# Kernel tuning notes

Hardware: AMD Instinct MI355X
Metric: run time of the kernel (lower is better)

## Reference

```python
import jax, jax.numpy as jnp
import numpy as np

B, S, H, NH, HD = 2, 2048, 4096, 32, 128
NEG = jnp.finfo(jnp.float32).min


def rotate_half(x):
    x1, x2 = x[..., : x.shape[-1] // 2], x[..., x.shape[-1] // 2 :]
    return jnp.concatenate((-x2, x1), axis=-1)


def setup_inputs() -> dict:
    key = jax.random.key(0)
    ks = jax.random.split(key, 7)
    return {
        "hidden_states": jax.random.normal(ks[0], (B, S, H), jnp.float32),
        "cos": jax.random.uniform(ks[1], (1, 1, S, HD), jnp.float32),
        "sin": jax.random.uniform(ks[2], (1, 1, S, HD), jnp.float32),
        "Wq": jax.random.normal(ks[3], (H, H), jnp.float32) * 0.02,
        "Wk": jax.random.normal(ks[4], (HD, H), jnp.float32) * 0.02,
        "Wv": jax.random.normal(ks[5], (HD, H), jnp.float32) * 0.02,
        "Wd": jax.random.normal(ks[6], (H, H), jnp.float32) * 0.02,
    }


def reference(hidden_states, cos, sin, Wq, Wk, Wv, Wd):
    b, s, _ = hidden_states.shape
    q = (hidden_states @ Wq.T).reshape(b, s, NH, HD).transpose(0, 2, 1, 3)  # [B,NH,S,HD]
    k = (hidden_states @ Wk.T)[:, None, :, :]  # [B,1,S,HD] (multi-query)
    v = (hidden_states @ Wv.T)[:, None, :, :]
    # inline RoPE
    q = q * cos + rotate_half(q) * sin
    k = k * cos + rotate_half(k) * sin
    scale = 1.0 / jnp.sqrt(jnp.float32(HD))
    scores = jnp.einsum("bhqd,bhkd->bhqk", q, k) * scale
    # causal mask: additive finfo.min above diagonal
    causal = jnp.tril(jnp.ones((s, s), jnp.bool_))
    scores = scores + jnp.where(causal, 0.0, NEG)
    attn = jax.nn.softmax(scores, axis=-1)
    out = jnp.einsum("bhqk,bhkd->bhqd", attn, v)  # [B,NH,S,HD]
    out = out.transpose(0, 2, 1, 3).reshape(b, s, NH * HD)
    return out @ Wd.T
```

## Files before the change

kernel.cpp:

```cpp
#include <hip/hip_runtime.h>
#include <hip/hip_bf16.h>
#include <math.h>

constexpr int Bc  = 2;
constexpr int Sc  = 2048;
constexpr int Hc  = 4096;
constexpr int NHc = 32;
constexpr int HDc = 128;

typedef __attribute__((ext_vector_type(8))) __bf16 bf16x8;
typedef __attribute__((ext_vector_type(4))) __bf16 bf16x4;
typedef __attribute__((ext_vector_type(4))) float  f32x4;

#if defined(__has_builtin)
#if __has_builtin(__builtin_amdgcn_global_load_lds)
#define HAS_GLL 1
#endif
#endif
#ifndef HAS_GLL
#define HAS_GLL 0
#endif

__device__ __forceinline__ float fast_exp2(float x) {
#if defined(__has_builtin)
#if __has_builtin(__builtin_amdgcn_exp2f)
    return __builtin_amdgcn_exp2f(x);
#else
    return exp2f(x);
#endif
#else
    return exp2f(x);
#endif
}

#define CFENCE asm volatile("" ::: "memory")
#define BARRIER do { CFENCE; __builtin_amdgcn_s_barrier(); CFENCE; } while (0)
#define WAITVM(n) asm volatile("s_waitcnt vmcnt(" #n ")" ::: "memory")

__device__ __forceinline__ void gll16(const __bf16* g, __bf16* lds_base, int lane) {
#if HAS_GLL
    __builtin_amdgcn_global_load_lds((const __attribute__((address_space(1))) void*)g,
                                     (__attribute__((address_space(3))) void*)lds_base,
                                     16, 0, 0);
#else
    *(int4*)(lds_base + lane * 8) = *(const int4*)g;
#endif
}

__global__ void cvt_f32_bf16(const float* __restrict__ in, __bf16* __restrict__ out, int n) {
    int i = (blockIdx.x * blockDim.x + threadIdx.x) * 4;
    if (i >= n) return;
    const float4 v = *(const float4*)(in + i);
    bf16x4 o;
    o[0] = (__bf16)v.x; o[1] = (__bf16)v.y; o[2] = (__bf16)v.z; o[3] = (__bf16)v.w;
    *(bf16x4*)(out + i) = o;
}

__global__ void prep(const float* __restrict__ hs, const float* __restrict__ Wq,
                     const float* __restrict__ Wk, const float* __restrict__ Wv,
                     __bf16* __restrict__ hs16, __bf16* __restrict__ wq16,
                     __bf16* __restrict__ wkv16) {
    const int blk = blockIdx.x;
    if (blk < 16384) {
        int i = (blk * 256 + threadIdx.x) * 4;
        const float4 v = *(const float4*)(hs + i);
        bf16x4 o;
        o[0] = (__bf16)v.x; o[1] = (__bf16)v.y; o[2] = (__bf16)v.z; o[3] = (__bf16)v.w;
        *(bf16x4*)(hs16 + i) = o;
    } else if (blk < 32768) {
        int i = ((blk - 16384) * 256 + threadIdx.x) * 4;
        const float4 v = *(const float4*)(Wq + i);
        bf16x4 o;
        o[0] = (__bf16)v.x; o[1] = (__bf16)v.y; o[2] = (__bf16)v.z; o[3] = (__bf16)v.w;
        *(bf16x4*)(wq16 + i) = o;
    } else {
        int i = ((blk - 32768) * 256 + threadIdx.x) * 4;
        int row = i >> 12;
        int col = i & (Hc - 1);
        const float* src = (row < HDc) ? (Wk + (long)row * Hc + col)
                                       : (Wv + (long)(row - HDc) * Hc + col);
        const float4 v = *(const float4*)src;
        bf16x4 o;
        o[0] = (__bf16)v.x; o[1] = (__bf16)v.y; o[2] = (__bf16)v.z; o[3] = (__bf16)v.w;
        *(bf16x4*)(wkv16 + i) = o;
    }
}

template <typename OUT>
__global__ __launch_bounds__(512, 2)
void gemm256(const __bf16* __restrict__ A, const __bf16* __restrict__ B,
             OUT* __restrict__ C, int M, int N, int K) {
    __shared__ __bf16 As[2][256 * 64];
    __shared__ __bf16 Bs[2][256 * 64];

    const int tid  = threadIdx.x;
    const int wave = tid >> 6, lane = tid & 63;
    const int lrow = lane & 15, quad = lane >> 4;
    const int wm = wave >> 2, wn = wave & 3;

    const int nwg = gridDim.x * gridDim.y;
    const int bid = blockIdx.y * gridDim.x + blockIdx.x;
    const int wg  = (bid & 7) * (nwg >> 3) + (bid >> 3);
    const int m0  = (wg / gridDim.x) * 256;
    const int n0  = (wg % gridDim.x) * 256;

    f32x4 acc[8][4] = {};

    int srow[4][2], sbase[4][2];
    const int rp   = lane >> 3;
    const int scol = ((lane & 7) ^ rp) << 3;
#pragma unroll
    for (int it = 0; it < 2; ++it) {
        const int c   = wave * 2 + it;
        const int rb0 = (c < 8) ? c * 8 : 128 + (c - 8) * 8;
        const int rb1 = (c >> 2) * 64 + (c & 3) * 8;
        srow[0][it] = rb0 + rp;       sbase[0][it] = rb0 * 64;
        srow[1][it] = rb1 + rp;       sbase[1][it] = rb1 * 64;
        srow[2][it] = rb1 + 32 + rp;  sbase[2][it] = (rb1 + 32) * 64;
        srow[3][it] = rb0 + 64 + rp;  sbase[3][it] = (rb0 + 64) * 64;
    }
    const __bf16* Ab = A + (long)m0 * K;
    const __bf16* Bb = B + (long)n0 * K;

    auto stageg = [&](int g, int bu, long k0) {
        const __bf16* gb = (g == 0 || g == 3) ? Ab : Bb;
        __bf16* lb = (g == 0 || g == 3) ? &As[bu][0] : &Bs[bu][0];
#pragma unroll
        for (int it = 0; it < 2; ++it)
            gll16(gb + (long)srow[g][it] * K + k0 + scol, lb + sbase[g][it], lane);
    };

    const int fc0  = ((quad ^ (lrow & 7)) << 3);
    const int fc1  = (((4 | quad) ^ (lrow & 7)) << 3);
    const int arow = wm * 128 + lrow;
    const int brow = wn * 64 + lrow;

    const int nk = K >> 6;
    stageg(0, 0, 0); stageg(1, 0, 0); stageg(2, 0, 0); stageg(3, 0, 0);
    WAITVM(4);
    BARRIER;

    for (int kt = 0; kt < nk; ++kt) {
        const int bu = kt & 1;
        const bool more = (kt + 1 < nk);
        const long k1 = (long)(kt + 1) * 64;
        bf16x8 af[2][4], bv0[2][2], bv1[2][2];

#pragma unroll
        for (int i2 = 0; i2 < 4; ++i2) {
            af[0][i2] = *(const bf16x8*)&As[bu][(arow + i2 * 16) * 64 + fc0];
            af[1][i2] = *(const bf16x8*)&As[bu][(arow + i2 * 16) * 64 + fc1];
        }
#pragma unroll
        for (int j2 = 0; j2 < 2; ++j2) {
            bv0[0][j2] = *(const bf16x8*)&Bs[bu][(brow + j2 * 16) * 64 + fc0];
            bv0[1][j2] = *(const bf16x8*)&Bs[bu][(brow + j2 * 16) * 64 + fc1];
        }
        if (more) { stageg(0, bu ^ 1, k1); WAITVM(4); } else { WAITVM(0); }
        BARRIER;
        __builtin_amdgcn_s_setprio(1);
#pragma unroll
        for (int c = 0; c < 2; ++c)
#pragma unroll
            for (int i2 = 0; i2 < 4; ++i2)
#pragma unroll
                for (int j2 = 0; j2 < 2; ++j2)
                    acc[i2][j2] = __builtin_amdgcn_mfma_f32_16x16x32_bf16(
                        af[c][i2], bv0[c][j2], acc[i2][j2], 0, 0, 0);
        __builtin_amdgcn_s_setprio(0);
        BARRIER;

#pragma unroll
        for (int j2 = 0; j2 < 2; ++j2) {
            bv1[0][j2] = *(const bf16x8*)&Bs[bu][(brow + 32 + j2 * 16) * 64 + fc0];
            bv1[1][j2] = *(const bf16x8*)&Bs[bu][(brow + 32 + j2 * 16) * 64 + fc1];
        }
        if (more) { stageg(1, bu ^ 1, k1); WAITVM(4); } else { WAITVM(0); }
        BARRIER;
        __builtin_amdgcn_s_setprio(1);
#pragma unroll
        for (int c = 0; c < 2; ++c)
#pragma unroll
            for (int i2 = 0; i2 < 4; ++i2)
#pragma unroll
                for (int j2 = 0; j2 < 2; ++j2)
                    acc[i2][2 + j2] = __builtin_amdgcn_mfma_f32_16x16x32_bf16(
                        af[c][i2], bv1[c][j2], acc[i2][2 + j2], 0, 0, 0);
        __builtin_amdgcn_s_setprio(0);
        BARRIER;

#pragma unroll
        for (int i2 = 0; i2 < 4; ++i2) {
            af[0][i2] = *(const bf16x8*)&As[bu][(arow + 64 + i2 * 16) * 64 + fc0];
            af[1][i2] = *(const bf16x8*)&As[bu][(arow + 64 + i2 * 16) * 64 + fc1];
        }
        if (more) { stageg(2, bu ^ 1, k1); WAITVM(4); } else { WAITVM(0); }
        BARRIER;
        __builtin_amdgcn_s_setprio(1);
#pragma unroll
        for (int c = 0; c < 2; ++c)
#pragma unroll
            for (int i2 = 0; i2 < 4; ++i2)
#pragma unroll
                for (int j2 = 0; j2 < 2; ++j2)
                    acc[4 + i2][j2] = __builtin_amdgcn_mfma_f32_16x16x32_bf16(
                        af[c][i2], bv0[c][j2], acc[4 + i2][j2], 0, 0, 0);
        __builtin_amdgcn_s_setprio(0);
        BARRIER;

        if (more) { stageg(3, bu ^ 1, k1); WAITVM(4); } else { WAITVM(0); }
        BARRIER;
        __builtin_amdgcn_s_setprio(1);
#pragma unroll
        for (int c = 0; c < 2; ++c)
#pragma unroll
            for (int i2 = 0; i2 < 4; ++i2)
#pragma unroll
                for (int j2 = 0; j2 < 2; ++j2)
                    acc[4 + i2][2 + j2] = __builtin_amdgcn_mfma_f32_16x16x32_bf16(
                        af[c][i2], bv1[c][j2], acc[4 + i2][2 + j2], 0, 0, 0);
        __builtin_amdgcn_s_setprio(0);
        BARRIER;
    }

#pragma unroll
    for (int i = 0; i < 8; ++i) {
        const int row = m0 + wm * 128 + i * 16 + quad * 4;
#pragma unroll
        for (int j = 0; j < 4; ++j) {
            const int col = n0 + wn * 64 + j * 16 + lrow;
            OUT* cp = C + (long)row * N + col;
#pragma unroll
            for (int r = 0; r < 4; ++r) cp[(long)r * N] = (OUT)acc[i][j][r];
        }
    }
}

template <typename OUT>
__global__ __launch_bounds__(256)
void gemm_bt64(const __bf16* __restrict__ A, const __bf16* __restrict__ B,
               OUT* __restrict__ C, int M, int N, int K) {
    __shared__ __bf16 As[2][64][64];
    __shared__ __bf16 Bs[2][64][64];

    const int tid  = threadIdx.x;
    const int wave = tid >> 6, lane = tid & 63;
    const int lrow = lane & 15, quad = lane >> 4;
    const int m0   = blockIdx.y * 64;
    const int n0   = blockIdx.x * 64;
    const int wr   = (wave >> 1) * 32;
    const int wc   = (wave & 1) * 32;

    f32x4 acc[2][2] = {};

    int srow[2], scol[2];
#pragma unroll
    for (int it = 0; it < 2; ++it) {
        int e = (wave * 2 + it) * 1024 + lane * 16;
        int r = e >> 7;
        int cb = (e >> 4) & 7;
        srow[it] = r;
        scol[it] = ((cb ^ (r & 7)) * 8);
    }
    const __bf16* Ab = A + (long)m0 * K;
    const __bf16* Bb = B + (long)n0 * K;

    auto stage = [&](int kt, int bu) {
        const long k0 = (long)kt * 64;
#pragma unroll
        for (int it = 0; it < 2; ++it)
            gll16(Ab + (long)srow[it] * K + k0 + scol[it], &As[bu][0][0] + (wave * 2 + it) * 512, lane);
#pragma unroll
        for (int it = 0; it < 2; ++it)
            gll16(Bb + (long)srow[it] * K + k0 + scol[it], &Bs[bu][0][0] + (wave * 2 + it) * 512, lane);
    };

    const int fcol0 = ((quad ^ (lrow & 7)) << 3);
    const int fcol1 = (((4 | quad) ^ (lrow & 7)) << 3);

    const int nk = K >> 6;
    stage(0, 0);
    for (int kt = 0; kt < nk; ++kt) {
        __syncthreads();
        if (kt + 1 < nk) stage(kt + 1, (kt + 1) & 1);
        const int bu = kt & 1;

#pragma unroll
        for (int c = 0; c < 2; ++c) {
            const int fc = c ? fcol1 : fcol0;
            bf16x8 af[2], bfv[2];
#pragma unroll
            for (int i = 0; i < 2; ++i) af[i]  = *(const bf16x8*)&As[bu][wr + i * 16 + lrow][fc];
#pragma unroll
            for (int j = 0; j < 2; ++j) bfv[j] = *(const bf16x8*)&Bs[bu][wc + j * 16 + lrow][fc];
#pragma unroll
            for (int i = 0; i < 2; ++i)
#pragma unroll
                for (int j = 0; j < 2; ++j)
                    acc[i][j] = __builtin_amdgcn_mfma_f32_16x16x32_bf16(af[i], bfv[j], acc[i][j], 0, 0, 0);
        }
    }

#pragma unroll
    for (int i = 0; i < 2; ++i) {
        const int row = m0 + wr + i * 16 + quad * 4;
#pragma unroll
        for (int j = 0; j < 2; ++j) {
            const int col = n0 + wc + j * 16 + lrow;
            OUT* cp = C + (long)row * N + col;
#pragma unroll
            for (int r = 0; r < 4; ++r) cp[(long)r * N] = (OUT)acc[i][j][r];
        }
    }
}

__global__ void ropek_vtrans(__bf16* __restrict__ KV, const float* __restrict__ cosb,
                             const float* __restrict__ sinb, __bf16* __restrict__ Vt) {
    __shared__ __bf16 T[128][72];
    const int tid = threadIdx.x;
    if (blockIdx.x < 128) {
        int gid  = blockIdx.x * 256 + tid;
        int row  = gid >> 3;
        int dblk = (gid & 7) * 8;
        int s    = row & (Sc - 1);
        __bf16* p = KV + (long)row * 256;
        const float* cp = cosb + s * HDc;
        const float* sp = sinb + s * HDc;
        bf16x8 lo = *(bf16x8*)(p + dblk);
        bf16x8 hi = *(bf16x8*)(p + dblk + 64);
        bf16x8 olo, ohi;
#pragma unroll
        for (int j = 0; j < 8; ++j) {
            float ql = (float)lo[j], qh = (float)hi[j];
            float cl = cp[dblk + j],      sl = sp[dblk + j];
            float ch = cp[dblk + 64 + j], sh = sp[dblk + 64 + j];
            olo[j] = (__bf16)(ql * cl - qh * sl);
            ohi[j] = (__bf16)(qh * ch + ql * sh);
        }
        *(bf16x8*)(p + dblk)      = olo;
        *(bf16x8*)(p + dblk + 64) = ohi;
    } else {
        const int vb = blockIdx.x - 128;
        const int s0 = (vb & (Sc / 64 - 1)) * 64;
        const int b  = vb / (Sc / 64);
#pragma unroll
        for (int i = 0; i < 4; ++i) {
            int e = i * 256 + tid;
            int s = e >> 4, dc = (e & 15) * 8;
            bf16x8 v = *(const bf16x8*)(KV + (long)(b * Sc + s0 + s) * 256 + 128 + dc);
#pragma unroll
            for (int j = 0; j < 8; ++j) T[dc + j][s] = v[j];
        }
        __syncthreads();
#pragma unroll
        for (int i = 0; i < 4; ++i) {
            int e = i * 256 + tid;
            int d = e >> 3, sc8 = (e & 7) * 8;
            bf16x8 v;
#pragma unroll
            for (int j = 0; j < 8; ++j) v[j] = T[d][sc8 + j];
            *(bf16x8*)(Vt + (long)(b * HDc + d) * Sc + s0 + sc8) = v;
        }
    }
}

__global__ __launch_bounds__(256, 2)
void attn(const __bf16* __restrict__ Q,
          const __bf16* __restrict__ KV,
          const __bf16* __restrict__ Vt,
          const float* __restrict__ cosb,
          const float* __restrict__ sinb,
          __bf16* __restrict__ O) {
    const int qt   = (gridDim.x - 1) - blockIdx.x;
    const int bh   = blockIdx.y;
    const int b    = bh >> 5, h = bh & 31;
    const int tid  = threadIdx.x;
    const int wave = tid >> 6, lane = tid & 63;
    const int lrow = lane & 15, quad = lane >> 4;

    __shared__ __bf16 Ks[2][64][128];
    __shared__ __bf16 Vs[2][128][64];
    __shared__ __bf16 Ps[4][16][72];

    bf16x8 vone;
#pragma unroll
    for (int j = 0; j < 8; ++j) vone[j] = (__bf16)1.0f;

    const int q0 = qt * 128 + wave * 32;

    const float qscale = 0.08838834764831845f * 1.4426950408889634f;
    bf16x8 aq[2][4];
#pragma unroll
    for (int qq = 0; qq < 2; ++qq) {
        const int s = q0 + qq * 16 + lrow;
        const __bf16* qp = Q + (long)(b * Sc + s) * Hc + h * HDc + quad * 8;
        const float* cp = cosb + s * HDc + quad * 8;
        const float* sp = sinb + s * HDc + quad * 8;
        bf16x8 raw[4];
#pragma unroll
        for (int c = 0; c < 4; ++c) raw[c] = *(const bf16x8*)(qp + c * 32);
#pragma unroll
        for (int c = 0; c < 2; ++c) {
#pragma unroll
            for (int j = 0; j < 8; ++j) {
                const int d = c * 32 + j;
                float ql = (float)raw[c][j], qh = (float)raw[c + 2][j];
                float cl = cp[d],      sl = sp[d];
                float ch = cp[d + 64], sh = sp[d + 64];
                aq[qq][c][j]     = (__bf16)((ql * cl - qh * sl) * qscale);
                aq[qq][c + 2][j] = (__bf16)((qh * ch + ql * sh) * qscale);
            }
        }
    }

    f32x4 o[2][8] = {};
    f32x4 lac[2] = {};
    float mst[2][4];
#pragma unroll
    for (int qq = 0; qq < 2; ++qq)
#pragma unroll
        for (int r = 0; r < 4; ++r) mst[qq][r] = -3.0e38f;

    const __bf16* kvb = KV + (long)b * Sc * 256;
    const __bf16* vtb = Vt + (long)b * HDc * Sc;
    int krow[4], kcol[4], vrow[4], vcol[4];
#pragma unroll
    for (int it = 0; it < 4; ++it) {
        int e = (wave * 4 + it) * 1024 + lane * 16;
        int rk = e >> 8, cbk = (e >> 4) & 15;
        krow[it] = rk; kcol[it] = ((cbk ^ (rk & 15)) * 8);
        int rv = e >> 7, cbv = (e >> 4) & 7;
        vrow[it] = rv; vcol[it] = ((cbv ^ (rv & 7)) * 8);
    }

    auto stage = [&](int kt, int bu) {
#pragma unroll
        for (int it = 0; it < 4; ++it) {
            gll16(kvb + (long)(kt * 64 + krow[it]) * 256 + kcol[it],
                  &Ks[bu][0][0] + (wave * 4 + it) * 512, lane);
            gll16(vtb + (long)vrow[it] * Sc + kt * 64 + vcol[it],
                  &Vs[bu][0][0] + (wave * 4 + it) * 512, lane);
        }
    };

    const int nt = 2 * qt + 2;
    stage(0, 0);

    for (int kt = 0; kt < nt; ++kt) {
        __syncthreads();
        if (kt + 1 < nt) stage(kt + 1, (kt + 1) & 1);
        const int bu = kt & 1;

        f32x4 sc[2][4] = {};
        __builtin_amdgcn_s_setprio(1);
#pragma unroll
        for (int ct = 0; ct < 4; ++ct) {
#pragma unroll
            for (int c = 0; c < 4; ++c) {
                bf16x8 bk = *(const bf16x8*)&Ks[bu][ct * 16 + lrow][(((c << 2) | quad) ^ lrow) << 3];
                sc[0][ct] = __builtin_amdgcn_mfma_f32_16x16x32_bf16(aq[0][c], bk, sc[0][ct], 0, 0, 0);
                sc[1][ct] = __builtin_amdgcn_mfma_f32_16x16x32_bf16(aq[1][c], bk, sc[1][ct], 0, 0, 0);
            }
        }
        __builtin_amdgcn_s_setprio(0);

        bf16x8 ap[2][2];
#pragma unroll
        for (int qq = 0; qq < 2; ++qq) {
            if (kt * 64 + 63 > q0 + qq * 16) {
#pragma unroll
                for (int ct = 0; ct < 4; ++ct) {
                    int kv = kt * 64 + ct * 16 + lrow;
#pragma unroll
                    for (int r = 0; r < 4; ++r) {
                        int qr = q0 + qq * 16 + quad * 4 + r;
                        if (kv > qr) sc[qq][ct][r] = -3.0e38f;
                    }
                }
            }

            float lmax[4];
#pragma unroll
            for (int r = 0; r < 4; ++r)
                lmax[r] = fmaxf(fmaxf(sc[qq][0][r], sc[qq][1][r]),
                                fmaxf(sc[qq][2][r], sc[qq][3][r]));
            const bool near_ok = (lmax[0] <= mst[qq][0] + 8.0f) &&
                                 (lmax[1] <= mst[qq][1] + 8.0f) &&
                                 (lmax[2] <= mst[qq][2] + 8.0f) &&
                                 (lmax[3] <= mst[qq][3] + 8.0f);
            if (!__all(near_ok)) {
                float alf[4];
#pragma unroll
                for (int r = 0; r < 4; ++r) {
                    float mx = lmax[r];
#pragma unroll
                    for (int off = 1; off < 16; off <<= 1) mx = fmaxf(mx, __shfl_xor(mx, off, 64));
                    float mnew = fmaxf(mst[qq][r], mx);
                    alf[r]     = fast_exp2(mst[qq][r] - mnew);
                    mst[qq][r] = mnew;
                }
#pragma unroll
                for (int dt = 0; dt < 8; ++dt)
#pragma unroll
                    for (int r = 0; r < 4; ++r) o[qq][dt][r] *= alf[r];
#pragma unroll
                for (int r = 0; r < 4; ++r) lac[qq][r] *= alf[r];
            }
#pragma unroll
            for (int ct = 0; ct < 4; ++ct)
#pragma unroll
                for (int r = 0; r < 4; ++r)
                    sc[qq][ct][r] = fast_exp2(sc[qq][ct][r] - mst[qq][r]);

#pragma unroll
            for (int ct = 0; ct < 4; ++ct)
#pragma unroll
                for (int r = 0; r < 4; ++r)
                    Ps[wave][quad * 4 + r][ct * 16 + lrow] = (__bf16)sc[qq][ct][r];
#pragma unroll
            for (int ks = 0; ks < 2; ++ks)
                ap[qq][ks] = *(const bf16x8*)&Ps[wave][lrow][ks * 32 + quad * 8];
        }

        __builtin_amdgcn_s_setprio(1);
#pragma unroll
        for (int dt = 0; dt < 8; ++dt) {
#pragma unroll
            for (int ks = 0; ks < 2; ++ks) {
                bf16x8 bv = *(const bf16x8*)&Vs[bu][dt * 16 + lrow]
                                [(((ks << 2) | quad) ^ (lrow & 7)) << 3];
#pragma unroll
                for (int qq = 0; qq < 2; ++qq)
                    o[qq][dt] = __builtin_amdgcn_mfma_f32_16x16x32_bf16(ap[qq][ks], bv, o[qq][dt], 0, 0, 0);
            }
        }
#pragma unroll
        for (int ks = 0; ks < 2; ++ks) {
#pragma unroll
            for (int qq = 0; qq < 2; ++qq)
                lac[qq] = __builtin_amdgcn_mfma_f32_16x16x32_bf16(ap[qq][ks], vone, lac[qq], 0, 0, 0);
        }
        __builtin_amdgcn_s_setprio(0);
    }

#pragma unroll
    for (int qq = 0; qq < 2; ++qq)
#pragma unroll
        for (int r = 0; r < 4; ++r) {
            float inv = 1.f / lac[qq][r];
            int qr = q0 + qq * 16 + quad * 4 + r;
            __bf16* op = O + (long)(b * Sc + qr) * Hc + h * HDc;
#pragma unroll
            for (int dt = 0; dt < 8; ++dt) op[dt * 16 + lrow] = (__bf16)(o[qq][dt][r] * inv);
        }
}

extern "C" void kernel_launch(void* const* d_in, const int* in_sizes, int n_in,
                              void* d_out, int out_size, void* d_ws, size_t ws_size,
                              hipStream_t stream) {
    const float* hs   = (const float*)d_in[0];
    const float* cosb = (const float*)d_in[1];
    const float* sinb = (const float*)d_in[2];
    const float* Wq   = (const float*)d_in[3];
    const float* Wk   = (const float*)d_in[4];
    const float* Wv   = (const float*)d_in[5];
    const float* Wd   = (const float*)d_in[6];
    float* out = (float*)d_out;

    char* ws = (char*)d_ws;
    const long SZ_HS  = (long)Bc * Sc * Hc * 2;
    const long SZ_W   = (long)Hc * Hc * 2;
    const long SZ_KV  = (long)Bc * Sc * 256 * 2;
    __bf16* hs16  = (__bf16*)(ws);
    __bf16* wq16  = (__bf16*)(ws + SZ_HS);
    __bf16* wkv16 = (__bf16*)(ws + SZ_HS + SZ_W);
    __bf16* q16   = (__bf16*)(ws + SZ_HS + SZ_W + SZ_KV);
    __bf16* kv16  = (__bf16*)(ws + SZ_HS + SZ_W + SZ_KV + SZ_HS);
    __bf16* vt16  = (__bf16*)(ws + SZ_HS + SZ_W + SZ_KV + SZ_HS + SZ_KV);
    __bf16* att16 = hs16;
    __bf16* wd16  = wq16;

    const int nW  = Hc * Hc;

    prep<<<33792, 256, 0, stream>>>(hs, Wq, Wk, Wv, hs16, wq16, wkv16);

    gemm256<__bf16><<<dim3(Hc / 256, (Bc * Sc) / 256), 512, 0, stream>>>(
        hs16, wq16, q16, Bc * Sc, Hc, Hc);
    gemm_bt64<__bf16><<<dim3(256 / 64, (Bc * Sc) / 64), 256, 0, stream>>>(
        hs16, wkv16, kv16, Bc * Sc, 256, Hc);

    cvt_f32_bf16<<<nW / 1024, 256, 0, stream>>>(Wd, wd16, nW);

    ropek_vtrans<<<128 + Bc * (Sc / 64), 256, 0, stream>>>(kv16, cosb, sinb, vt16);

    attn<<<dim3(Sc / 128, Bc * NHc), 256, 0, stream>>>(q16, kv16, vt16, cosb, sinb, att16);

    gemm256<float><<<dim3(Hc / 256, (Bc * Sc) / 256), 512, 0, stream>>>(
        att16, wd16, out, Bc * Sc, Hc, Hc);
}
```

Baseline: 654.6 us.

## Fuse Q and KV projections into one 256-tile GEMM and fold Wd cast into prep

The separate small-tile KV projection GEMM is merged into the large-tile Q GEMM by appending the 256 KV output columns as an extra N-tile column, with per-block output pointer and stride selection. When the workspace is large enough, Wd is converted to bf16 inside the prep kernel into its own buffer instead of a separate launch that reuses the Wq buffer. This removes two launches and the poorly-occupied 64x64 GEMM. The cost is a grid of 17 N-tiles that the swizzle remapping may handle unevenly, plus extra workspace.

After: 741.4 us. 1.13x slower.

```diff
diff --git a/kernel.cpp b/kernel.cpp
--- a/kernel.cpp
+++ b/kernel.cpp
@@ -58,8 +58,9 @@
 
 __global__ void prep(const float* __restrict__ hs, const float* __restrict__ Wq,
                      const float* __restrict__ Wk, const float* __restrict__ Wv,
+                     const float* __restrict__ Wd,
                      __bf16* __restrict__ hs16, __bf16* __restrict__ wq16,
-                     __bf16* __restrict__ wkv16) {
+                     __bf16* __restrict__ wkv16, __bf16* __restrict__ wd16) {
     const int blk = blockIdx.x;
     if (blk < 16384) {
         int i = (blk * 256 + threadIdx.x) * 4;
@@ -73,7 +74,7 @@
         bf16x4 o;
         o[0] = (__bf16)v.x; o[1] = (__bf16)v.y; o[2] = (__bf16)v.z; o[3] = (__bf16)v.w;
         *(bf16x4*)(wq16 + i) = o;
-    } else {
+    } else if (blk < 33792) {
         int i = ((blk - 32768) * 256 + threadIdx.x) * 4;
         int row = i >> 12;
         int col = i & (Hc - 1);
@@ -83,13 +84,19 @@
         bf16x4 o;
         o[0] = (__bf16)v.x; o[1] = (__bf16)v.y; o[2] = (__bf16)v.z; o[3] = (__bf16)v.w;
         *(bf16x4*)(wkv16 + i) = o;
-    }
-}
-
-template <typename OUT>
+    } else {
+        int i = ((blk - 33792) * 256 + threadIdx.x) * 4;
+        const float4 v = *(const float4*)(Wd + i);
+        bf16x4 o;
+        o[0] = (__bf16)v.x; o[1] = (__bf16)v.y; o[2] = (__bf16)v.z; o[3] = (__bf16)v.w;
+        *(bf16x4*)(wd16 + i) = o;
+    }
+}
+
 __global__ __launch_bounds__(512, 2)
-void gemm256(const __bf16* __restrict__ A, const __bf16* __restrict__ B,
-             OUT* __restrict__ C, int M, int N, int K) {
+void gemm_qkv(const __bf16* __restrict__ A, const __bf16* __restrict__ Wq16,
+              const __bf16* __restrict__ Wkv16, __bf16* __restrict__ Qo,
+              __bf16* __restrict__ KVo, int M, int K) {
     __shared__ __bf16 As[2][256 * 64];
     __shared__ __bf16 Bs[2][256 * 64];
 
@@ -120,7 +127,8 @@
         srow[3][it] = rb0 + 64 + rp;  sbase[3][it] = (rb0 + 64) * 64;
     }
     const __bf16* Ab = A + (long)m0 * K;
-    const __bf16* Bb = B + (long)n0 * K;
+    const __bf16* Bb = (n0 < Hc) ? (Wq16 + (long)n0 * K)
+                                 : (Wkv16 + (long)(n0 - Hc) * K);
 
     auto stageg = [&](int g, int bu, long k0) {
         const __bf16* gb = (g == 0 || g == 3) ? Ab : Bb;
@@ -223,90 +231,165 @@
         BARRIER;
     }
 
+    const long ldc  = (n0 < Hc) ? Hc : 256;
+    const int  nloc = (n0 < Hc) ? n0 : n0 - Hc;
+    __bf16* Cb = (n0 < Hc) ? Qo : KVo;
 #pragma unroll
     for (int i = 0; i < 8; ++i) {
         const int row = m0 + wm * 128 + i * 16 + quad * 4;
 #pragma unroll
         for (int j = 0; j < 4; ++j) {
-            const int col = n0 + wn * 64 + j * 16 + lrow;
-            OUT* cp = C + (long)row * N + col;
-#pragma unroll
-            for (int r = 0; r < 4; ++r) cp[(long)r * N] = (OUT)acc[i][j][r];
+            const int col = nloc + wn * 64 + j * 16 + lrow;
+            __bf16* cp = Cb + (long)row * ldc + col;
+#pragma unroll
+            for (int r = 0; r < 4; ++r) cp[(long)r * ldc] = (__bf16)acc[i][j][r];
         }
     }
 }
 
 template <typename OUT>
-__global__ __launch_bounds__(256)
-void gemm_bt64(const __bf16* __restrict__ A, const __bf16* __restrict__ B,
-               OUT* __restrict__ C, int M, int N, int K) {
-    __shared__ __bf16 As[2][64][64];
-    __shared__ __bf16 Bs[2][64][64];
+__global__ __launch_bounds__(512, 2)
+void gemm256(const __bf16* __restrict__ A, const __bf16* __restrict__ B,
+             OUT* __restrict__ C, int M, int N, int K) {
+    __shared__ __bf16 As[2][256 * 64];
+    __shared__ __bf16 Bs[2][256 * 64];
 
     const int tid  = threadIdx.x;
     const int wave = tid >> 6, lane = tid & 63;
     const int lrow = lane & 15, quad = lane >> 4;
-    const int m0   = blockIdx.y * 64;
-    const int n0   = blockIdx.x * 64;
-    const int wr   = (wave >> 1) * 32;
-    const int wc   = (wave & 1) * 32;
-
-    f32x4 acc[2][2] = {};
-
-    int srow[2], scol[2];
+    const int wm = wave >> 2, wn = wave & 3;
+
+    const int nwg = gridDim.x * gridDim.y;
+    const int bid = blockIdx.y * gridDim.x + blockIdx.x;
+    const int wg  = (bid & 7) * (nwg >> 3) + (bid >> 3);
+    const int m0  = (wg / gridDim.x) * 256;
+    const int n0  = (wg % gridDim.x) * 256;
+
+    f32x4 acc[8][4] = {};
+
+    int srow[4][2], sbase[4][2];
+    const int rp   = lane >> 3;
+    const int scol = ((lane & 7) ^ rp) << 3;
 #pragma unroll
     for (int it = 0; it < 2; ++it) {
-        int e = (wave * 2 + it) * 1024 + lane * 16;
-        int r = e >> 7;
-        int cb = (e >> 4) & 7;
-        srow[it] = r;
-        scol[it] = ((cb ^ (r & 7)) * 8);
+        const int c   = wave * 2 + it;
+        const int rb0 = (c < 8) ? c * 8 : 128 + (c - 8) * 8;
+        const int rb1 = (c >> 2) * 64 + (c & 3) * 8;
+        srow[0][it] = rb0 + rp;       sbase[0][it] = rb0 * 64;
+        srow[1][it] = rb1 + rp;       sbase[1][it] = rb1 * 64;
+        srow[2][it] = rb1 + 32 + rp;  sbase[2][it] = (rb1 + 32) * 64;
+        srow[3][it] = rb0 + 64 + rp;  sbase[3][it] = (rb0 + 64) * 64;
     }
     const __bf16* Ab = A + (long)m0 * K;
     const __bf16* Bb = B + (long)n0 * K;
 
-    auto stage = [&](int kt, int bu) {
-        const long k0 = (long)kt * 64;
+    auto stageg = [&](int g, int bu, long k0) {
+        const __bf16* gb = (g == 0 || g == 3) ? Ab : Bb;
+        __bf16* lb = (g == 0 || g == 3) ? &As[bu][0] : &Bs[bu][0];
 #pragma unroll
         for (int it = 0; it < 2; ++it)
-            gll16(Ab + (long)srow[it] * K + k0 + scol[it], &As[bu][0][0] + (wave * 2 + it) * 512, lane);
-#pragma unroll
-        for (int it = 0; it < 2; ++it)
-            gll16(Bb + (long)srow[it] * K + k0 + scol[it], &Bs[bu][0][0] + (wave * 2 + it) * 512, lane);
+            gll16(gb + (long)srow[g][it] * K + k0 + scol, lb + sbase[g][it], lane);
     };
 
-    const int fcol0 = ((quad ^ (lrow & 7)) << 3);
-    const int fcol1 = (((4 | quad) ^ (lrow & 7)) << 3);
+    const int fc0  = ((quad ^ (lrow & 7)) << 3);
+    const int fc1  = (((4 | quad) ^ (lrow & 7)) << 3);
+    const int arow = wm * 128 + lrow;
+    const int brow = wn * 64 + lrow;
 
     const int nk = K >> 6;
-    stage(0, 0);
+    stageg(0, 0, 0); stageg(1, 0, 0); stageg(2, 0, 0); stageg(3, 0, 0);
+    WAITVM(4);
+    BARRIER;
+
     for (int kt = 0; kt < nk; ++kt) {
-        __syncthreads();
-        if (kt + 1 < nk) stage(kt + 1, (kt + 1) & 1);
         const int bu = kt & 1;
-
-#pragma unroll
-        for (int c = 0; c < 2; ++c) {
-            const int fc = c ? fcol1 : fcol0;
-            bf16x8 af[2], bfv[2];
-#pragma unroll
-            for (int i = 0; i < 2; ++i) af[i]  = *(const bf16x8*)&As[bu][wr + i * 16 + lrow][fc];
-#pragma unroll
-            for (int j = 0; j < 2; ++j) bfv[j] = *(const bf16x8*)&Bs[bu][wc + j * 16 + lrow][fc];
-#pragma unroll
-            for (int i = 0; i < 2; ++i)
-#pragma unroll
-                for (int j = 0; j < 2; ++j)
-                    acc[i][j] = __builtin_amdgcn_mfma_f32_16x16x32_bf16(af[i], bfv[j], acc[i][j], 0, 0, 0);
-        }
-    }
-
-#pragma unroll
-    for (int i = 0; i < 2; ++i) {
-        const int row = m0 + wr + i * 16 + quad * 4;
-#pragma unroll
-        for (int j = 0; j < 2; ++j) {
-            const int col = n0 + wc + j * 16 + lrow;
+        const bool more = (kt + 1 < nk);
+        const long k1 = (long)(kt + 1) * 64;
+        bf16x8 af[2][4], bv0[2][2], bv1[2][2];
+
+#pragma unroll
+        for (int i2 = 0; i2 < 4; ++i2) {
+            af[0][i2] = *(const bf16x8*)&As[bu][(arow + i2 * 16) * 64 + fc0];
+            af[1][i2] = *(const bf16x8*)&As[bu][(arow + i2 * 16) * 64 + fc1];
+        }
+#pragma unroll
+        for (int j2 = 0; j2 < 2; ++j2) {
+            bv0[0][j2] = *(const bf16x8*)&Bs[bu][(brow + j2 * 16) * 64 + fc0];
+            bv0[1][j2] = *(const bf16x8*)&Bs[bu][(brow + j2 * 16) * 64 + fc1];
+        }
+        if (more) { stageg(0, bu ^ 1, k1); WAITVM(4); } else { WAITVM(0); }
+        BARRIER;
+        __builtin_amdgcn_s_setprio(1);
+#pragma unroll
+        for (int c = 0; c < 2; ++c)
+#pragma unroll
+            for (int i2 = 0; i2 < 4; ++i2)
+#pragma unroll
+                for (int j2 = 0; j2 < 2; ++j2)
+                    acc[i2][j2] = __builtin_amdgcn_mfma_f32_16x16x32_bf16(
+                        af[c][i2], bv0[c][j2], acc[i2][j2], 0, 0, 0);
+        __builtin_amdgcn_s_setprio(0);
+        BARRIER;
+
+#pragma unroll
+        for (int j2 = 0; j2 < 2; ++j2) {
+            bv1[0][j2] = *(const bf16x8*)&Bs[bu][(brow + 32 + j2 * 16) * 64 + fc0];
+            bv1[1][j2] = *(const bf16x8*)&Bs[bu][(brow + 32 + j2 * 16) * 64 + fc1];
+        }
+        if (more) { stageg(1, bu ^ 1, k1); WAITVM(4); } else { WAITVM(0); }
+        BARRIER;
+        __builtin_amdgcn_s_setprio(1);
+#pragma unroll
+        for (int c = 0; c < 2; ++c)
+#pragma unroll
+            for (int i2 = 0; i2 < 4; ++i2)
+#pragma unroll
+                for (int j2 = 0; j2 < 2; ++j2)
+                    acc[i2][2 + j2] = __builtin_amdgcn_mfma_f32_16x16x32_bf16(
+                        af[c][i2], bv1[c][j2], acc[i2][2 + j2], 0, 0, 0);
+        __builtin_amdgcn_s_setprio(0);
+        BARRIER;
+
+#pragma unroll
+        for (int i2 = 0; i2 < 4; ++i2) {
+            af[0][i2] = *(const bf16x8*)&As[bu][(arow + 64 + i2 * 16) * 64 + fc0];
+            af[1][i2] = *(const bf16x8*)&As[bu][(arow + 64 + i2 * 16) * 64 + fc1];
+        }
+        if (more) { stageg(2, bu ^ 1, k1); WAITVM(4); } else { WAITVM(0); }
+        BARRIER;
+        __builtin_amdgcn_s_setprio(1);
+#pragma unroll
+        for (int c = 0; c < 2; ++c)
+#pragma unroll
+            for (int i2 = 0; i2 < 4; ++i2)
+#pragma unroll
+                for (int j2 = 0; j2 < 2; ++j2)
+                    acc[4 + i2][j2] = __builtin_amdgcn_mfma_f32_16x16x32_bf16(
+                        af[c][i2], bv0[c][j2], acc[4 + i2][j2], 0, 0, 0);
+        __builtin_amdgcn_s_setprio(0);
+        BARRIER;
+
+        if (more) { stageg(3, bu ^ 1, k1); WAITVM(4); } else { WAITVM(0); }
+        BARRIER;
+        __builtin_amdgcn_s_setprio(1);
+#pragma unroll
+        for (int c = 0; c < 2; ++c)
+#pragma unroll
+            for (int i2 = 0; i2 < 4; ++i2)
+#pragma unroll
+                for (int j2 = 0; j2 < 2; ++j2)
+                    acc[4 + i2][2 + j2] = __builtin_amdgcn_mfma_f32_16x16x32_bf16(
+                        af[c][i2], bv1[c][j2], acc[4 + i2][2 + j2], 0, 0, 0);
+        __builtin_amdgcn_s_setprio(0);
+        BARRIER;
+    }
+
+#pragma unroll
+    for (int i = 0; i < 8; ++i) {
+        const int row = m0 + wm * 128 + i * 16 + quad * 4;
+#pragma unroll
+        for (int j = 0; j < 4; ++j) {
+            const int col = n0 + wn * 64 + j * 16 + lrow;
             OUT* cp = C + (long)row * N + col;
 #pragma unroll
             for (int r = 0; r < 4; ++r) cp[(long)r * N] = (OUT)acc[i][j][r];
@@ -571,6 +654,7 @@
     const long SZ_HS  = (long)Bc * Sc * Hc * 2;
     const long SZ_W   = (long)Hc * Hc * 2;
     const long SZ_KV  = (long)Bc * Sc * 256 * 2;
+    const long SZ_VT  = (long)Bc * HDc * Sc * 2;
     __bf16* hs16  = (__bf16*)(ws);
     __bf16* wq16  = (__bf16*)(ws + SZ_HS);
     __bf16* wkv16 = (__bf16*)(ws + SZ_HS + SZ_W);
@@ -578,18 +662,21 @@
     __bf16* kv16  = (__bf16*)(ws + SZ_HS + SZ_W + SZ_KV + SZ_HS);
     __bf16* vt16  = (__bf16*)(ws + SZ_HS + SZ_W + SZ_KV + SZ_HS + SZ_KV);
     __bf16* att16 = hs16;
-    __bf16* wd16  = wq16;
-
-    const int nW  = Hc * Hc;
-
-    prep<<<33792, 256, 0, stream>>>(hs, Wq, Wk, Wv, hs16, wq16, wkv16);
-
-    gemm256<__bf16><<<dim3(Hc / 256, (Bc * Sc) / 256), 512, 0, stream>>>(
-        hs16, wq16, q16, Bc * Sc, Hc, Hc);
-    gemm_bt64<__bf16><<<dim3(256 / 64, (Bc * Sc) / 64), 256, 0, stream>>>(
-        hs16, wkv16, kv16, Bc * Sc, 256, Hc);
-
-    cvt_f32_bf16<<<nW / 1024, 256, 0, stream>>>(Wd, wd16, nW);
+
+    const long base = SZ_HS + SZ_W + SZ_KV + SZ_HS + SZ_KV + SZ_VT;
+    const bool sepwd = ws_size >= (size_t)(base + SZ_W);
+    __bf16* wd16 = sepwd ? (__bf16*)(ws + base) : wq16;
+
+    const int nW = Hc * Hc;
+
+    prep<<<sepwd ? 50176 : 33792, 256, 0, stream>>>(
+        hs, Wq, Wk, Wv, Wd, hs16, wq16, wkv16, wd16);
+
+    gemm_qkv<<<dim3((Hc + 256) / 256, (Bc * Sc) / 256), 512, 0, stream>>>(
+        hs16, wq16, wkv16, q16, kv16, Bc * Sc, Hc);
+
+    if (!sepwd)
+        cvt_f32_bf16<<<nW / 1024, 256, 0, stream>>>(Wd, wd16, nW);
 
     ropek_vtrans<<<128 + Bc * (Sc / 64), 256, 0, stream>>>(kv16, cosb, sinb, vt16);
 
```
